# Optimization experiments

Measured on AMD Instinct MI355X. Metric: run time of the kernel, lower is better.

The kernel has to match this reference:

```python
import jax, jax.numpy as jnp
import numpy as np

NUM_HEADS = 16
THETA = 1000.0


def apply_rope(x, positions, theta):
    """x: [B, H, S, d_k]; positions: [S] float. Interleaved-pair RoPE."""
    d = x.shape[-1]
    inv_freq = theta ** (-jnp.arange(0, d, 2, dtype=x.dtype) / d)  # [d/2]
    ang = positions[:, None] * inv_freq[None, :]                    # [S, d/2]
    cos, sin = jnp.cos(ang), jnp.sin(ang)
    x1, x2 = x[..., 0::2], x[..., 1::2]
    r1 = x1 * cos - x2 * sin
    r2 = x1 * sin + x2 * cos
    return jnp.stack([r1, r2], axis=-1).reshape(x.shape)


def setup_inputs() -> dict:
    key = jax.random.key(0)
    ks = jax.random.split(key, 5)
    B, S, D = 2, 2048, 1024
    scale = 1.0 / np.sqrt(D)
    return {
        "in_features": jax.random.normal(ks[0], (B, S, D), jnp.float32),
        "q_proj_weight": jax.random.normal(ks[1], (D, D), jnp.float32) * scale,
        "k_proj_weight": jax.random.normal(ks[2], (D, D), jnp.float32) * scale,
        "v_proj_weight": jax.random.normal(ks[3], (D, D), jnp.float32) * scale,
        "o_proj_weight": jax.random.normal(ks[4], (D, D), jnp.float32) * scale,
        "token_positions": jnp.arange(S, dtype=jnp.int32),
    }


def reference(in_features, q_proj_weight, k_proj_weight, v_proj_weight,
              o_proj_weight, token_positions):
    B, S, D = in_features.shape
    H = NUM_HEADS
    d_k = D // H

    # Original rearrange: '(d_k heads) d_model -> heads d_model d_k'
    # => first dim splits as [d_k, heads] (heads is the inner factor).
    def split_heads(w):
        return w.reshape(d_k, H, D).transpose(1, 2, 0)  # [H, D, d_k]

    Wq, Wk, Wv = split_heads(q_proj_weight), split_heads(k_proj_weight), split_heads(v_proj_weight)

    xq = jnp.einsum("bsd,hdk->bhsk", in_features, Wq)
    xk = jnp.einsum("bsd,hdk->bhsk", in_features, Wk)
    xv = jnp.einsum("bsd,hdk->bhsk", in_features, Wv)

    pos = token_positions.astype(in_features.dtype)
    xq = apply_rope(xq, pos, THETA)
    xk = apply_rope(xk, pos, THETA)

    scores = jnp.einsum("bhqk,bhmk->bhqm", xq, xk) / jnp.sqrt(
        jnp.asarray(d_k, in_features.dtype))
    causal_mask = jnp.triu(jnp.ones((S, S), bool), k=1)  # True above diagonal
    scores = jnp.where(causal_mask, -jnp.inf, scores)
    attn = jax.nn.softmax(scores, axis=-1)

    out = jnp.einsum("bhqm,bhmv->bhqv", attn, xv)        # [B, H, S, d_k]
    out = out.transpose(0, 2, 1, 3).reshape(B, S, D)     # (heads d_emb) concat
    return out @ o_proj_weight                            # [B, S, d_o]
```

## Files before the change

### kernel.cpp

```cpp
#include <hip/hip_runtime.h>

typedef unsigned short u16;
typedef unsigned int u32;
typedef __bf16 bf16x8 __attribute__((ext_vector_type(8)));
typedef float f32x4 __attribute__((ext_vector_type(4)));

#define SEQ 2048
#define DMODEL 1024
#define NH 16
#define DK 64
#define BATCH 2
#define MTOT (BATCH * SEQ)

__device__ __forceinline__ u16 f2b(float f) {
  u32 u = __float_as_uint(f);
  u += 0x7fffu + ((u >> 16) & 1u);
  return (u16)(u >> 16);
}

__device__ __forceinline__ void gload16(const void* g, void* l) {
  __builtin_amdgcn_global_load_lds((const __attribute__((address_space(1))) u32*)g,
                                   (__attribute__((address_space(3))) u32*)l, 16, 0, 0);
}

__global__ __launch_bounds__(256) void cvt_bf16(const float* __restrict__ in,
                                                u16* __restrict__ out, int n4) {
  int i = blockIdx.x * 256 + threadIdx.x;
  if (i < n4) {
    float4 v = ((const float4*)in)[i];
    uint2 o;
    o.x = (u32)f2b(v.x) | ((u32)f2b(v.y) << 16);
    o.y = (u32)f2b(v.z) | ((u32)f2b(v.w) << 16);
    ((uint2*)out)[i] = o;
  }
}

__global__ __launch_bounds__(256) void cvt_w3(const float* __restrict__ wq,
                                              const float* __restrict__ wk,
                                              const float* __restrict__ wv,
                                              u16* __restrict__ oq,
                                              u16* __restrict__ ok,
                                              u16* __restrict__ ov) {
  const int m = blockIdx.y;
  const float* in = (m == 0) ? wq : ((m == 1) ? wk : wv);
  u16* out = (m == 0) ? oq : ((m == 1) ? ok : ov);
  const int i = blockIdx.x * 256 + threadIdx.x;
  float4 v = ((const float4*)in)[i];
  uint2 o;
  o.x = (u32)f2b(v.x) | ((u32)f2b(v.y) << 16);
  o.y = (u32)f2b(v.z) | ((u32)f2b(v.w) << 16);
  ((uint2*)out)[i] = o;
}

__global__ __launch_bounds__(256) void rope_tab_k(const int* __restrict__ tokpos,
                                                  float2* __restrict__ tab) {
  const int i = blockIdx.x * 256 + threadIdx.x;
  const int s = i >> 5, Xi = i & 31;
  const float invf = powf(1000.0f, -(float)Xi / 32.0f);
  const float ang = (float)tokpos[s] * invf;
  float sn, cs;
  sincosf(ang, &sn, &cs);
  tab[i] = make_float2(cs, sn);
}

__global__ __launch_bounds__(256) void transpose_wo(const float* __restrict__ wo,
                                                    u16* __restrict__ wot) {
  __shared__ float tile[32][33];
  const int bx = blockIdx.x * 32;
  const int by = blockIdx.y * 32;
  const int tx = threadIdx.x & 31, ty = threadIdx.x >> 5;
  for (int j = ty; j < 32; j += 8)
    tile[j][tx] = wo[(size_t)(by + j) * DMODEL + bx + tx];
  __syncthreads();
  for (int j = ty; j < 32; j += 8)
    wot[(size_t)(bx + j) * DMODEL + by + tx] = f2b(tile[tx][j]);
}

template <int MI>
__device__ __forceinline__ void gemm_core(const u16* __restrict__ A,
                                          const u16* __restrict__ Bt,
                                          int mbase, int nbase,
                                          u16* As, u16* Bs, f32x4 acc[MI][4]) {
  const int t = threadIdx.x;
  const int lane = t & 63, w = t >> 6;
  const int wr = w >> 1, wc = w & 1;
  const int l15 = lane & 15, lg = lane >> 4;
  const int srow = t >> 3;
  const int sch = (t & 7) ^ (srow & 7);
  const int rsw = l15 & 7;
  const int ASZ = MI * 32 * 64;
  const int BSZ = 128 * 64;
  const int NIT = DMODEL / 64;

  auto stage = [&](int bufsel, int kb) {
    u16* Ad = &As[bufsel * ASZ];
    u16* Bd = &Bs[bufsel * BSZ];
#pragma unroll
    for (int j = 0; j < MI; ++j)
      gload16(&A[(size_t)(mbase + srow + 32 * j) * DMODEL + kb + sch * 8],
              &Ad[j * 2048 + t * 8]);
#pragma unroll
    for (int j = 0; j < 4; ++j)
      gload16(&Bt[(size_t)(nbase + srow + 32 * j) * DMODEL + kb + sch * 8],
              &Bd[j * 2048 + t * 8]);
  };

  auto compute = [&](int bufsel) {
    const u16* Ac = &As[bufsel * ASZ];
    const u16* Bc = &Bs[bufsel * BSZ];
#pragma unroll
    for (int kk = 0; kk < 2; ++kk) {
      bf16x8 af[MI], bfr[4];
#pragma unroll
      for (int mi = 0; mi < MI; ++mi) {
        const int row = wr * (MI * 16) + mi * 16 + l15;
        af[mi] = *(const bf16x8*)&Ac[row * 64 + (((kk * 4 + lg) ^ rsw) * 8)];
      }
#pragma unroll
      for (int ni = 0; ni < 4; ++ni) {
        const int row = wc * 64 + ni * 16 + l15;
        bfr[ni] = *(const bf16x8*)&Bc[row * 64 + (((kk * 4 + lg) ^ rsw) * 8)];
      }
#pragma unroll
      for (int mi = 0; mi < MI; ++mi)
#pragma unroll
        for (int ni = 0; ni < 4; ++ni)
          acc[mi][ni] =
              __builtin_amdgcn_mfma_f32_16x16x32_bf16(af[mi], bfr[ni], acc[mi][ni], 0, 0, 0);
    }
  };

  stage(0, 0);

  for (int it = 0; it < NIT - 1; ++it) {
    const int buf = it & 1;
    stage(buf ^ 1, (it + 1) * 64);
    __builtin_amdgcn_sched_barrier(0);
    if constexpr (MI == 4) {
      asm volatile("s_waitcnt vmcnt(8)" ::: "memory");
    } else {
      asm volatile("s_waitcnt vmcnt(6)" ::: "memory");
    }
    __builtin_amdgcn_sched_barrier(0);
    __builtin_amdgcn_s_barrier();
    __builtin_amdgcn_sched_barrier(0);
    compute(buf);
    __builtin_amdgcn_sched_barrier(0);
    __builtin_amdgcn_s_barrier();
  }
  asm volatile("s_waitcnt vmcnt(0)" ::: "memory");
  __builtin_amdgcn_sched_barrier(0);
  __builtin_amdgcn_s_barrier();
  __builtin_amdgcn_sched_barrier(0);
  compute((NIT - 1) & 1);
}

__global__ __launch_bounds__(256) void gemm_qkv(
    const u16* __restrict__ Xb, const u16* __restrict__ Wqb,
    const u16* __restrict__ Wkb, const u16* __restrict__ Wvb,
    u16* __restrict__ Qb, u16* __restrict__ Kb, u16* __restrict__ Vb,
    const float2* __restrict__ tab) {
  __shared__ __align__(16) u16 As[2 * 128 * 64];
  __shared__ __align__(16) u16 Bs[2 * 128 * 64];

  const int mat = blockIdx.y >> 3;
  const int nbase = (blockIdx.y & 7) * 128;
  const int mbase = blockIdx.x * 128;
  const u16* Bt = (mat == 0) ? Wqb : ((mat == 1) ? Wkb : Wvb);

  f32x4 acc[4][4];
#pragma unroll
  for (int mi = 0; mi < 4; ++mi)
#pragma unroll
    for (int ni = 0; ni < 4; ++ni) {
      f32x4 z = {0.f, 0.f, 0.f, 0.f};
      acc[mi][ni] = z;
    }

  gemm_core<4>(Xb, Bt, mbase, nbase, As, Bs, acc);

  const int t = threadIdx.x;
  const int lane = t & 63, w = t >> 6;
  const int wr = w >> 1, wc = w & 1;
  const int l15 = lane & 15, lg = lane >> 4;

  if (mat == 2) {
#pragma unroll
    for (int mi = 0; mi < 4; ++mi) {
#pragma unroll
      for (int r = 0; r < 4; ++r) {
        const int row = mbase + wr * 64 + mi * 16 + lg * 4 + r;
        const int bi = row >> 11, s = row & (SEQ - 1);
#pragma unroll
        for (int ni = 0; ni < 4; ++ni) {
          const int c = nbase + wc * 64 + ni * 16 + l15;
          const int hh = c & 15, vd = c >> 4;
          Vb[((size_t)((bi * NH + hh) * DK + vd)) * SEQ + s] = f2b(acc[mi][ni][r]);
        }
      }
    }
  } else {
    u16* Ob = (mat == 0) ? Qb : Kb;
    const float qscale = (mat == 0) ? 0.125f * 1.44269504088896f : 1.0f;
#pragma unroll
    for (int ni = 0; ni < 4; ni += 2) {
      const int Xi = (nbase + wc * 64 + ni * 16) >> 5;
#pragma unroll
      for (int mi = 0; mi < 4; ++mi) {
#pragma unroll
        for (int r = 0; r < 4; ++r) {
          const int row = mbase + wr * 64 + mi * 16 + lg * 4 + r;
          const int bi = row >> 11, s = row & (SEQ - 1);
          const float2 ct = tab[(s << 5) + Xi];
          const float x1 = acc[mi][ni][r], x2 = acc[mi][ni + 1][r];
          const float r1 = (x1 * ct.x - x2 * ct.y) * qscale;
          const float r2 = (x1 * ct.y + x2 * ct.x) * qscale;
          const u32 pk = (u32)f2b(r1) | ((u32)f2b(r2) << 16);
          *(u32*)&Ob[((size_t)((bi * NH + l15) * SEQ + s) << 6) + (Xi << 1)] = pk;
        }
      }
    }
  }
}

__global__ __launch_bounds__(256) void flash_attn(
    const u16* __restrict__ Qg, const u16* __restrict__ Kg,
    const u16* __restrict__ VTg, u16* __restrict__ Ag) {
  __shared__ __align__(16) u16 Ks[2][64 * 64];
  __shared__ __align__(16) u16 Vs[2][64 * 64];
  __shared__ __align__(16) u16 Ps[4][16][72];

  const int id = blockIdx.y * 32 + blockIdx.x;
  const int within = id >> 3;
  const int bh = (id & 7) * 4 + (within & 3);
  const int qt = 31 - (within >> 2);
  const int b = bh >> 4, h = bh & 15;
  const int qbase = qt * 64;

  const size_t hoff = (size_t)bh * SEQ * DK;
  const u16* Qh = Qg + hoff;
  const u16* Kh = Kg + hoff;
  const u16* VTh = VTg + hoff;

  const int t = threadIdx.x;
  const int lane = t & 63, w = t >> 6;
  const int l15 = lane & 15, lg = lane >> 4;
  const int sw = l15 & 7;

  const int qrow = qbase + w * 16 + l15;
  const bf16x8 qf0 = *(const bf16x8*)&Qh[(size_t)qrow * DK + lg * 8];
  const bf16x8 qf1 = *(const bf16x8*)&Qh[(size_t)qrow * DK + 32 + lg * 8];

  f32x4 oaccT[4];
#pragma unroll
  for (int vf = 0; vf < 4; ++vf) {
    f32x4 z = {0.f, 0.f, 0.f, 0.f};
    oaccT[vf] = z;
  }
  float m_r = -1e30f, l_r = 0.0f;

  const int srow = t >> 3;
  const int sc = ((t & 7) ^ (srow & 7)) * 8;

  gload16(&Kh[(size_t)srow * DK + sc], &Ks[0][t * 8]);
  gload16(&Kh[(size_t)(srow + 32) * DK + sc], &Ks[0][2048 + t * 8]);
  gload16(&VTh[(size_t)srow * SEQ + sc], &Vs[0][t * 8]);
  gload16(&VTh[(size_t)(srow + 32) * SEQ + sc], &Vs[0][2048 + t * 8]);

  for (int kt = 0; kt <= qt; ++kt) {
    const int buf = kt & 1;
    __syncthreads();
    if (kt < qt) {
      const int kb = (kt + 1) * 64;
      gload16(&Kh[(size_t)(kb + srow) * DK + sc], &Ks[buf ^ 1][t * 8]);
      gload16(&Kh[(size_t)(kb + srow + 32) * DK + sc], &Ks[buf ^ 1][2048 + t * 8]);
      gload16(&VTh[(size_t)srow * SEQ + kb + sc], &Vs[buf ^ 1][t * 8]);
      gload16(&VTh[(size_t)(srow + 32) * SEQ + kb + sc], &Vs[buf ^ 1][2048 + t * 8]);
    }
    const int kvbase = kt * 64;

    f32x4 sT[4];
#pragma unroll
    for (int f = 0; f < 4; ++f) {
      const int row = f * 16 + l15;
      bf16x8 k0 = *(const bf16x8*)&Ks[buf][row * 64 + (lg ^ sw) * 8];
      bf16x8 k1 = *(const bf16x8*)&Ks[buf][row * 64 + ((4 + lg) ^ sw) * 8];
      f32x4 z = {0.f, 0.f, 0.f, 0.f};
      z = __builtin_amdgcn_mfma_f32_16x16x32_bf16(k0, qf0, z, 0, 0, 0);
      z = __builtin_amdgcn_mfma_f32_16x16x32_bf16(k1, qf1, z, 0, 0, 0);
      sT[f] = z;
    }

    if (kt == qt) {
#pragma unroll
      for (int f = 0; f < 4; ++f)
#pragma unroll
        for (int r = 0; r < 4; ++r) {
          const int kvc = kvbase + f * 16 + lg * 4 + r;
          if (kvc > qrow) sT[f][r] = -1e30f;
        }
    }

    f32x4 mv;
#pragma unroll
    for (int r = 0; r < 4; ++r)
      mv[r] = fmaxf(fmaxf(sT[0][r], sT[1][r]), fmaxf(sT[2][r], sT[3][r]));
    float mx = fmaxf(fmaxf(mv[0], mv[1]), fmaxf(mv[2], mv[3]));
    mx = fmaxf(mx, __shfl_xor(mx, 16));
    mx = fmaxf(mx, __shfl_xor(mx, 32));

    const float mn = fmaxf(m_r, mx);
    const float alpha = exp2f(m_r - mn);
    m_r = mn;
#pragma unroll
    for (int f = 0; f < 4; ++f)
#pragma unroll
      for (int r = 0; r < 4; ++r) sT[f][r] = exp2f(sT[f][r] - mn);

    f32x4 rv;
#pragma unroll
    for (int r = 0; r < 4; ++r) rv[r] = (sT[0][r] + sT[1][r]) + (sT[2][r] + sT[3][r]);
    float rs = (rv[0] + rv[1]) + (rv[2] + rv[3]);
    rs += __shfl_xor(rs, 16);
    rs += __shfl_xor(rs, 32);
    l_r = l_r * alpha + rs;

#pragma unroll
    for (int vf = 0; vf < 4; ++vf)
#pragma unroll
      for (int r = 0; r < 4; ++r) oaccT[vf][r] *= alpha;

#pragma unroll
    for (int f = 0; f < 4; ++f) {
      uint2 pkv;
      pkv.x = (u32)f2b(sT[f][0]) | ((u32)f2b(sT[f][1]) << 16);
      pkv.y = (u32)f2b(sT[f][2]) | ((u32)f2b(sT[f][3]) << 16);
      *(uint2*)&Ps[w][l15][f * 16 + lg * 4] = pkv;
    }

#pragma unroll
    for (int c = 0; c < 2; ++c) {
      const bf16x8 pb = *(const bf16x8*)&Ps[w][l15][c * 32 + lg * 8];
#pragma unroll
      for (int vf = 0; vf < 4; ++vf) {
        const bf16x8 va =
            *(const bf16x8*)&Vs[buf][(vf * 16 + l15) * 64 + ((c * 4 + lg) ^ sw) * 8];
        oaccT[vf] = __builtin_amdgcn_mfma_f32_16x16x32_bf16(va, pb, oaccT[vf], 0, 0, 0);
      }
    }
  }

  const float inv = 1.0f / l_r;
  const size_t base = ((size_t)(b * SEQ + qrow)) * DMODEL + h * DK;
#pragma unroll
  for (int vf = 0; vf < 4; ++vf) {
    uint2 ov;
    ov.x = (u32)f2b(oaccT[vf][0] * inv) | ((u32)f2b(oaccT[vf][1] * inv) << 16);
    ov.y = (u32)f2b(oaccT[vf][2] * inv) | ((u32)f2b(oaccT[vf][3] * inv) << 16);
    *(uint2*)&Ag[base + vf * 16 + lg * 4] = ov;
  }
}

__global__ __launch_bounds__(256) void gemm_out(const u16* __restrict__ Ab,
                                                const u16* __restrict__ Wotb,
                                                float* __restrict__ Co) {
  __shared__ __align__(16) u16 As[2 * 64 * 64];
  __shared__ __align__(16) u16 Bs[2 * 128 * 64];
  const int mbase = blockIdx.x * 64, nbase = blockIdx.y * 128;

  f32x4 acc[2][4];
#pragma unroll
  for (int mi = 0; mi < 2; ++mi)
#pragma unroll
    for (int ni = 0; ni < 4; ++ni) {
      f32x4 z = {0.f, 0.f, 0.f, 0.f};
      acc[mi][ni] = z;
    }

  gemm_core<2>(Ab, Wotb, mbase, nbase, As, Bs, acc);

  const int t = threadIdx.x;
  const int lane = t & 63, w = t >> 6;
  const int wr = w >> 1, wc = w & 1;
  const int l15 = lane & 15, lg = lane >> 4;
#pragma unroll
  for (int mi = 0; mi < 2; ++mi) {
#pragma unroll
    for (int r = 0; r < 4; ++r) {
      const int row = mbase + wr * 32 + mi * 16 + lg * 4 + r;
#pragma unroll
      for (int ni = 0; ni < 4; ++ni) {
        const int c = nbase + wc * 64 + ni * 16 + l15;
        Co[(size_t)row * DMODEL + c] = acc[mi][ni][r];
      }
    }
  }
}

extern "C" void kernel_launch(void* const* d_in, const int* in_sizes, int n_in,
                              void* d_out, int out_size, void* d_ws, size_t ws_size,
                              hipStream_t stream) {
  const float* X = (const float*)d_in[0];
  const float* Wq = (const float*)d_in[1];
  const float* Wk = (const float*)d_in[2];
  const float* Wv = (const float*)d_in[3];
  const float* Wo = (const float*)d_in[4];
  const int* tokpos = (const int*)d_in[5];
  float* out = (float*)d_out;

  u16* p = (u16*)d_ws;
  u16* Xb = p;   p += (size_t)MTOT * DMODEL;
  u16* Wqb = p;  p += (size_t)DMODEL * DMODEL;
  u16* Wkb = p;  p += (size_t)DMODEL * DMODEL;
  u16* Wvb = p;  p += (size_t)DMODEL * DMODEL;
  u16* Wotb = p; p += (size_t)DMODEL * DMODEL;
  u16* Qb = p;   p += (size_t)BATCH * NH * SEQ * DK;
  u16* Kb = p;   p += (size_t)BATCH * NH * SEQ * DK;
  u16* Vb = p;   p += (size_t)BATCH * NH * SEQ * DK;
  float2* tab = (float2*)(p + 512);
  u16* Ab = Xb;

  cvt_bf16<<<4096, 256, 0, stream>>>(X, Xb, (MTOT * DMODEL) / 4);
  cvt_w3<<<dim3(1024, 3), 256, 0, stream>>>(Wq, Wk, Wv, Wqb, Wkb, Wvb);
  transpose_wo<<<dim3(32, 32), 256, 0, stream>>>(Wo, Wotb);
  rope_tab_k<<<(SEQ * 32) / 256, 256, 0, stream>>>(tokpos, tab);

  gemm_qkv<<<dim3(32, 24), 256, 0, stream>>>(Xb, Wqb, Wkb, Wvb, Qb, Kb, Vb, tab);
  flash_attn<<<dim3(32, 32), 256, 0, stream>>>(Qb, Kb, Vb, Ab);
  gemm_out<<<dim3(64, 8), 256, 0, stream>>>(Ab, Wotb, out);
}
```

Baseline: 142.2 us.

## Retile QKV GEMM to 256x256 tiles with 512 threads and XCD-aware block remap

The QKV projection now uses one 512-thread block per 256x256 output tile, reading a single concatenated weight buffer (Wq, Wk and Wv are contiguous in the workspace). Block ids are remapped so consecutive tiles land on the same XCD, to improve L2 reuse. Larger tiles raise arithmetic intensity per LDS load and cut redundant global reads. The trade-off is only 192 blocks on a 256-CU part, plus higher register and LDS pressure (128KB LDS, 128 accumulator floats per thread). The output GEMM inlines the former shared core with identical logic.

After: 152.9 us. 1.08x slower.

```diff
diff --git a/kernel.cpp b/kernel.cpp
--- a/kernel.cpp
+++ b/kernel.cpp
@@ -76,44 +76,59 @@
     wot[(size_t)(bx + j) * DMODEL + by + tx] = f2b(tile[tx][j]);
 }
 
-template <int MI>
-__device__ __forceinline__ void gemm_core(const u16* __restrict__ A,
-                                          const u16* __restrict__ Bt,
-                                          int mbase, int nbase,
-                                          u16* As, u16* Bs, f32x4 acc[MI][4]) {
+__global__ __launch_bounds__(512) void gemm_qkv(
+    const u16* __restrict__ Xb, const u16* __restrict__ Wqkv,
+    u16* __restrict__ Qb, u16* __restrict__ Kb, u16* __restrict__ Vb,
+    const float2* __restrict__ tab) {
+  __shared__ __align__(16) u16 As[2 * 256 * 64];
+  __shared__ __align__(16) u16 Bs[2 * 256 * 64];
+
+  const int orig = blockIdx.y * 16 + blockIdx.x;
+  const int wgid = (orig & 7) * 24 + (orig >> 3);
+  const int mtile = wgid & 15, ntile = wgid >> 4;
+  const int mbase = mtile * 256;
+  const int nglob = ntile * 256;
+
   const int t = threadIdx.x;
   const int lane = t & 63, w = t >> 6;
-  const int wr = w >> 1, wc = w & 1;
+  const int wr = w >> 2, wc = w & 3;
   const int l15 = lane & 15, lg = lane >> 4;
   const int srow = t >> 3;
   const int sch = (t & 7) ^ (srow & 7);
   const int rsw = l15 & 7;
-  const int ASZ = MI * 32 * 64;
-  const int BSZ = 128 * 64;
-  const int NIT = DMODEL / 64;
+  const int BUF = 256 * 64;
+
+  f32x4 acc[8][4];
+#pragma unroll
+  for (int mi = 0; mi < 8; ++mi)
+#pragma unroll
+    for (int ni = 0; ni < 4; ++ni) {
+      f32x4 z = {0.f, 0.f, 0.f, 0.f};
+      acc[mi][ni] = z;
+    }
 
   auto stage = [&](int bufsel, int kb) {
-    u16* Ad = &As[bufsel * ASZ];
-    u16* Bd = &Bs[bufsel * BSZ];
-#pragma unroll
-    for (int j = 0; j < MI; ++j)
-      gload16(&A[(size_t)(mbase + srow + 32 * j) * DMODEL + kb + sch * 8],
-              &Ad[j * 2048 + t * 8]);
+    u16* Ad = &As[bufsel * BUF];
+    u16* Bd = &Bs[bufsel * BUF];
 #pragma unroll
     for (int j = 0; j < 4; ++j)
-      gload16(&Bt[(size_t)(nbase + srow + 32 * j) * DMODEL + kb + sch * 8],
-              &Bd[j * 2048 + t * 8]);
+      gload16(&Xb[(size_t)(mbase + j * 64 + srow) * DMODEL + kb + sch * 8],
+              &Ad[j * 4096 + t * 8]);
+#pragma unroll
+    for (int j = 0; j < 4; ++j)
+      gload16(&Wqkv[(size_t)(nglob + j * 64 + srow) * DMODEL + kb + sch * 8],
+              &Bd[j * 4096 + t * 8]);
   };
 
   auto compute = [&](int bufsel) {
-    const u16* Ac = &As[bufsel * ASZ];
-    const u16* Bc = &Bs[bufsel * BSZ];
+    const u16* Ac = &As[bufsel * BUF];
+    const u16* Bc = &Bs[bufsel * BUF];
 #pragma unroll
     for (int kk = 0; kk < 2; ++kk) {
-      bf16x8 af[MI], bfr[4];
-#pragma unroll
-      for (int mi = 0; mi < MI; ++mi) {
-        const int row = wr * (MI * 16) + mi * 16 + l15;
+      bf16x8 af[8], bfr[4];
+#pragma unroll
+      for (int mi = 0; mi < 8; ++mi) {
+        const int row = wr * 128 + mi * 16 + l15;
         af[mi] = *(const bf16x8*)&Ac[row * 64 + (((kk * 4 + lg) ^ rsw) * 8)];
       }
 #pragma unroll
@@ -122,7 +137,7 @@
         bfr[ni] = *(const bf16x8*)&Bc[row * 64 + (((kk * 4 + lg) ^ rsw) * 8)];
       }
 #pragma unroll
-      for (int mi = 0; mi < MI; ++mi)
+      for (int mi = 0; mi < 8; ++mi)
 #pragma unroll
         for (int ni = 0; ni < 4; ++ni)
           acc[mi][ni] =
@@ -132,15 +147,12 @@
 
   stage(0, 0);
 
+  const int NIT = DMODEL / 64;
   for (int it = 0; it < NIT - 1; ++it) {
     const int buf = it & 1;
     stage(buf ^ 1, (it + 1) * 64);
     __builtin_amdgcn_sched_barrier(0);
-    if constexpr (MI == 4) {
-      asm volatile("s_waitcnt vmcnt(8)" ::: "memory");
-    } else {
-      asm volatile("s_waitcnt vmcnt(6)" ::: "memory");
-    }
+    asm volatile("s_waitcnt vmcnt(8)" ::: "memory");
     __builtin_amdgcn_sched_barrier(0);
     __builtin_amdgcn_s_barrier();
     __builtin_amdgcn_sched_barrier(0);
@@ -153,48 +165,21 @@
   __builtin_amdgcn_s_barrier();
   __builtin_amdgcn_sched_barrier(0);
   compute((NIT - 1) & 1);
-}
-
-__global__ __launch_bounds__(256) void gemm_qkv(
-    const u16* __restrict__ Xb, const u16* __restrict__ Wqb,
-    const u16* __restrict__ Wkb, const u16* __restrict__ Wvb,
-    u16* __restrict__ Qb, u16* __restrict__ Kb, u16* __restrict__ Vb,
-    const float2* __restrict__ tab) {
-  __shared__ __align__(16) u16 As[2 * 128 * 64];
-  __shared__ __align__(16) u16 Bs[2 * 128 * 64];
-
-  const int mat = blockIdx.y >> 3;
-  const int nbase = (blockIdx.y & 7) * 128;
-  const int mbase = blockIdx.x * 128;
-  const u16* Bt = (mat == 0) ? Wqb : ((mat == 1) ? Wkb : Wvb);
-
-  f32x4 acc[4][4];
-#pragma unroll
-  for (int mi = 0; mi < 4; ++mi)
-#pragma unroll
-    for (int ni = 0; ni < 4; ++ni) {
-      f32x4 z = {0.f, 0.f, 0.f, 0.f};
-      acc[mi][ni] = z;
-    }
-
-  gemm_core<4>(Xb, Bt, mbase, nbase, As, Bs, acc);
-
-  const int t = threadIdx.x;
-  const int lane = t & 63, w = t >> 6;
-  const int wr = w >> 1, wc = w & 1;
-  const int l15 = lane & 15, lg = lane >> 4;
+
+  const int mat = ntile >> 2;
+  const int nb4 = ntile & 3;
 
   if (mat == 2) {
 #pragma unroll
-    for (int mi = 0; mi < 4; ++mi) {
+    for (int mi = 0; mi < 8; ++mi) {
 #pragma unroll
       for (int r = 0; r < 4; ++r) {
-        const int row = mbase + wr * 64 + mi * 16 + lg * 4 + r;
+        const int row = mbase + wr * 128 + mi * 16 + lg * 4 + r;
         const int bi = row >> 11, s = row & (SEQ - 1);
 #pragma unroll
         for (int ni = 0; ni < 4; ++ni) {
-          const int c = nbase + wc * 64 + ni * 16 + l15;
-          const int hh = c & 15, vd = c >> 4;
+          const int cm = nb4 * 256 + wc * 64 + ni * 16 + l15;
+          const int hh = cm & 15, vd = cm >> 4;
           Vb[((size_t)((bi * NH + hh) * DK + vd)) * SEQ + s] = f2b(acc[mi][ni][r]);
         }
       }
@@ -204,12 +189,12 @@
     const float qscale = (mat == 0) ? 0.125f * 1.44269504088896f : 1.0f;
 #pragma unroll
     for (int ni = 0; ni < 4; ni += 2) {
-      const int Xi = (nbase + wc * 64 + ni * 16) >> 5;
-#pragma unroll
-      for (int mi = 0; mi < 4; ++mi) {
+      const int Xi = (nb4 * 256 + wc * 64 + ni * 16) >> 5;
+#pragma unroll
+      for (int mi = 0; mi < 8; ++mi) {
 #pragma unroll
         for (int r = 0; r < 4; ++r) {
-          const int row = mbase + wr * 64 + mi * 16 + lg * 4 + r;
+          const int row = mbase + wr * 128 + mi * 16 + lg * 4 + r;
           const int bi = row >> 11, s = row & (SEQ - 1);
           const float2 ct = tab[(s << 5) + Xi];
           const float x1 = acc[mi][ni][r], x2 = acc[mi][ni + 1][r];
@@ -368,21 +353,80 @@
   __shared__ __align__(16) u16 Bs[2 * 128 * 64];
   const int mbase = blockIdx.x * 64, nbase = blockIdx.y * 128;
 
-  f32x4 acc[2][4];
-#pragma unroll
-  for (int mi = 0; mi < 2; ++mi)
-#pragma unroll
-    for (int ni = 0; ni < 4; ++ni) {
-      f32x4 z = {0.f, 0.f, 0.f, 0.f};
-      acc[mi][ni] = z;
-    }
-
-  gemm_core<2>(Ab, Wotb, mbase, nbase, As, Bs, acc);
-
   const int t = threadIdx.x;
   const int lane = t & 63, w = t >> 6;
   const int wr = w >> 1, wc = w & 1;
   const int l15 = lane & 15, lg = lane >> 4;
+  const int srow = t >> 3;
+  const int sch = (t & 7) ^ (srow & 7);
+  const int rsw = l15 & 7;
+  const int ASZ = 64 * 64, BSZ = 128 * 64;
+
+  f32x4 acc[2][4];
+#pragma unroll
+  for (int mi = 0; mi < 2; ++mi)
+#pragma unroll
+    for (int ni = 0; ni < 4; ++ni) {
+      f32x4 z = {0.f, 0.f, 0.f, 0.f};
+      acc[mi][ni] = z;
+    }
+
+  auto stage = [&](int bufsel, int kb) {
+    u16* Ad = &As[bufsel * ASZ];
+    u16* Bd = &Bs[bufsel * BSZ];
+    gload16(&Ab[(size_t)(mbase + srow) * DMODEL + kb + sch * 8], &Ad[t * 8]);
+    gload16(&Ab[(size_t)(mbase + 32 + srow) * DMODEL + kb + sch * 8], &Ad[2048 + t * 8]);
+#pragma unroll
+    for (int j = 0; j < 4; ++j)
+      gload16(&Wotb[(size_t)(nbase + srow + 32 * j) * DMODEL + kb + sch * 8],
+              &Bd[j * 2048 + t * 8]);
+  };
+
+  auto compute = [&](int bufsel) {
+    const u16* Ac = &As[bufsel * ASZ];
+    const u16* Bc = &Bs[bufsel * BSZ];
+#pragma unroll
+    for (int kk = 0; kk < 2; ++kk) {
+      bf16x8 af[2], bfr[4];
+#pragma unroll
+      for (int mi = 0; mi < 2; ++mi) {
+        const int row = wr * 32 + mi * 16 + l15;
+        af[mi] = *(const bf16x8*)&Ac[row * 64 + (((kk * 4 + lg) ^ rsw) * 8)];
+      }
+#pragma unroll
+      for (int ni = 0; ni < 4; ++ni) {
+        const int row = wc * 64 + ni * 16 + l15;
+        bfr[ni] = *(const bf16x8*)&Bc[row * 64 + (((kk * 4 + lg) ^ rsw) * 8)];
+      }
+#pragma unroll
+      for (int mi = 0; mi < 2; ++mi)
+#pragma unroll
+        for (int ni = 0; ni < 4; ++ni)
+          acc[mi][ni] =
+              __builtin_amdgcn_mfma_f32_16x16x32_bf16(af[mi], bfr[ni], acc[mi][ni], 0, 0, 0);
+    }
+  };
+
+  stage(0, 0);
+  const int NIT = DMODEL / 64;
+  for (int it = 0; it < NIT - 1; ++it) {
+    const int buf = it & 1;
+    stage(buf ^ 1, (it + 1) * 64);
+    __builtin_amdgcn_sched_barrier(0);
+    asm volatile("s_waitcnt vmcnt(6)" ::: "memory");
+    __builtin_amdgcn_sched_barrier(0);
+    __builtin_amdgcn_s_barrier();
+    __builtin_amdgcn_sched_barrier(0);
+    compute(buf);
+    __builtin_amdgcn_sched_barrier(0);
+    __builtin_amdgcn_s_barrier();
+  }
+  asm volatile("s_waitcnt vmcnt(0)" ::: "memory");
+  __builtin_amdgcn_sched_barrier(0);
+  __builtin_amdgcn_s_barrier();
+  __builtin_amdgcn_sched_barrier(0);
+  compute((NIT - 1) & 1);
+
 #pragma unroll
   for (int mi = 0; mi < 2; ++mi) {
 #pragma unroll
@@ -425,7 +469,7 @@
   transpose_wo<<<dim3(32, 32), 256, 0, stream>>>(Wo, Wotb);
   rope_tab_k<<<(SEQ * 32) / 256, 256, 0, stream>>>(tokpos, tab);
 
-  gemm_qkv<<<dim3(32, 24), 256, 0, stream>>>(Xb, Wqb, Wkb, Wvb, Qb, Kb, Vb, tab);
+  gemm_qkv<<<dim3(16, 12), 512, 0, stream>>>(Xb, Wqb, Qb, Kb, Vb, tab);
   flash_attn<<<dim3(32, 32), 256, 0, stream>>>(Qb, Kb, Vb, Ab);
   gemm_out<<<dim3(64, 8), 256, 0, stream>>>(Ab, Wotb, out);
 }
```
